# Performance work log

Measured on AMD Instinct MI355X. Metric: run time of the kernel, lower is better.

## Reference

```python
import jax, jax.numpy as jnp
import numpy as np

D_MODEL = 2048
N_HEADS = 16
D_HEAD = D_MODEL // N_HEADS
D_FF = 8192
EPS = 1e-6
ROPE_BASE = 10000.0


def rmsnorm(x, g):
    return x * jax.lax.rsqrt(jnp.mean(x * x, axis=-1, keepdims=True) + EPS) * g


def rotate_half(x):
    x1, x2 = jnp.split(x, 2, axis=-1)
    return jnp.concatenate((-x2, x1), axis=-1)


def rope_tables(T):
    inv_freq = 1.0 / (ROPE_BASE ** (jnp.arange(0, D_HEAD, 2, dtype=jnp.float32) / D_HEAD))
    freqs = jnp.arange(T, dtype=jnp.float32)[:, None] * inv_freq[None, :]  # [T, D_HEAD//2]
    emb = jnp.concatenate((freqs, freqs), axis=-1)  # [T, D_HEAD]
    return jnp.cos(emb), jnp.sin(emb)


def setup_inputs() -> dict:
    key = jax.random.key(0)
    ks = jax.random.split(key, 6)
    std = 0.02
    x = jax.random.normal(ks[0], (2, 2048, D_MODEL), dtype=jnp.float32)
    # weights stored (in, out) so forward is x @ W
    w_qkv = jax.random.normal(ks[1], (D_MODEL, 3 * D_MODEL), dtype=jnp.float32) * std
    w_out = jax.random.normal(ks[2], (D_MODEL, D_MODEL), dtype=jnp.float32) * std
    w_g = jax.random.normal(ks[3], (D_MODEL, D_FF), dtype=jnp.float32) * std
    w_u = jax.random.normal(ks[4], (D_MODEL, D_FF), dtype=jnp.float32) * std
    w_o = jax.random.normal(ks[5], (D_FF, D_MODEL), dtype=jnp.float32) * std
    g1 = jnp.ones((D_MODEL,), dtype=jnp.float32)
    g2 = jnp.ones((D_MODEL,), dtype=jnp.float32)
    return {"x": x, "w_qkv": w_qkv, "w_out": w_out, "g1": g1, "g2": g2,
            "w_g": w_g, "w_u": w_u, "w_o": w_o}


def reference(x, w_qkv, w_out, g1, g2, w_g, w_u, w_o):
    B, T, D = x.shape
    H, dh = N_HEADS, D_HEAD
    scale = dh ** -0.5

    h = rmsnorm(x, g1)
    qkv = h @ w_qkv  # [B, T, 3D]
    q, k, v = jnp.split(qkv, 3, axis=-1)
    # [B, H, T, dh]
    q = q.reshape(B, T, H, dh).transpose(0, 2, 1, 3)
    k = k.reshape(B, T, H, dh).transpose(0, 2, 1, 3)
    v = v.reshape(B, T, H, dh).transpose(0, 2, 1, 3)

    cos, sin = rope_tables(T)  # [T, dh] each
    cos = cos[None, None]
    sin = sin[None, None]
    q = q * cos + rotate_half(q) * sin
    k = k * cos + rotate_half(k) * sin

    scores = jnp.einsum('bhqd,bhkd->bhqk', q, k) * scale
    causal = jnp.arange(T)[None, :] <= jnp.arange(T)[:, None]  # [T, T]
    scores = jnp.where(causal[None, None], scores, -jnp.inf)
    attn = jax.nn.softmax(scores, axis=-1)
    ctx = jnp.einsum('bhqk,bhkd->bhqd', attn, v)  # [B, H, T, dh]
    ctx = ctx.transpose(0, 2, 1, 3).reshape(B, T, D)
    x = x + ctx @ w_out

    h = rmsnorm(x, g2)
    x = x + (jax.nn.silu(h @ w_g) * (h @ w_u)) @ w_o
    return x
```

## Files before the change

kernel.cpp:

```cpp
#include <hip/hip_runtime.h>

typedef __bf16 bf16x8 __attribute__((ext_vector_type(8)));
typedef float f32x4 __attribute__((ext_vector_type(4)));
typedef unsigned short u16x8 __attribute__((ext_vector_type(8)));

#define B_SZ 2
#define T_SEQ 2048
#define D_MODEL 2048
#define N_HEADS 16
#define D_HEAD 128
#define D_FF 8192
#define BT (B_SZ * T_SEQ)
#define NT (T_SEQ / 64)

__device__ __forceinline__ unsigned short f2bf(float f) {
  unsigned int u = __builtin_bit_cast(unsigned int, f);
  u += 0x7FFFu + ((u >> 16) & 1u);
  return (unsigned short)(u >> 16);
}
__device__ __forceinline__ float bf2f(unsigned short h) {
  unsigned int u = ((unsigned int)h) << 16;
  return __builtin_bit_cast(float, u);
}

__device__ __forceinline__ void load_lds16(const void* g, void* l) {
  __builtin_amdgcn_global_load_lds(
      (const __attribute__((address_space(1))) unsigned int*)g,
      (__attribute__((address_space(3))) unsigned int*)l, 16, 0, 0);
}

template <int N>
__device__ __forceinline__ void vm_gate() {
  if constexpr (N <= 0)
    asm volatile("s_waitcnt vmcnt(0)" ::: "memory");
  else if constexpr (N == 2)
    asm volatile("s_waitcnt vmcnt(2)" ::: "memory");
  else if constexpr (N == 3)
    asm volatile("s_waitcnt vmcnt(3)" ::: "memory");
  else if constexpr (N == 4)
    asm volatile("s_waitcnt vmcnt(4)" ::: "memory");
  else if constexpr (N == 6)
    asm volatile("s_waitcnt vmcnt(6)" ::: "memory");
  else
    asm volatile("s_waitcnt vmcnt(8)" ::: "memory");
}

__global__ __launch_bounds__(256) void transpose_cast_kernel(
    const float* __restrict__ in, unsigned short* __restrict__ out, int R, int C) {
  __shared__ float tile[32][33];
  const int tx = threadIdx.x, ty = threadIdx.y;
  const int c0 = blockIdx.x * 32, r0 = blockIdx.y * 32;
#pragma unroll
  for (int i = 0; i < 4; ++i)
    tile[ty + 8 * i][tx] = in[(long)(r0 + ty + 8 * i) * C + c0 + tx];
  __syncthreads();
#pragma unroll
  for (int i = 0; i < 4; ++i)
    out[(long)(c0 + ty + 8 * i) * R + r0 + tx] = f2bf(tile[tx][ty + 8 * i]);
}

__global__ __launch_bounds__(256) void rmsnorm_cast_kernel(
    const float* __restrict__ x, const float* __restrict__ gw,
    unsigned short* __restrict__ out) {
  const int row = blockIdx.x;
  const int tid = threadIdx.x;
  const float* xr = x + (long)row * D_MODEL;
  float4 a = *(const float4*)(xr + tid * 8);
  float4 b = *(const float4*)(xr + tid * 8 + 4);
  float ss = a.x * a.x + a.y * a.y + a.z * a.z + a.w * a.w +
             b.x * b.x + b.y * b.y + b.z * b.z + b.w * b.w;
#pragma unroll
  for (int d = 1; d < 64; d <<= 1) ss += __shfl_xor(ss, d);
  __shared__ float part[4];
  if ((tid & 63) == 0) part[tid >> 6] = ss;
  __syncthreads();
  ss = part[0] + part[1] + part[2] + part[3];
  const float rs = rsqrtf(ss * (1.0f / D_MODEL) + 1e-6f);
  float4 g0 = *(const float4*)(gw + tid * 8);
  float4 g1 = *(const float4*)(gw + tid * 8 + 4);
  ushort4 o0, o1;
  o0.x = f2bf(a.x * rs * g0.x); o0.y = f2bf(a.y * rs * g0.y);
  o0.z = f2bf(a.z * rs * g0.z); o0.w = f2bf(a.w * rs * g0.w);
  o1.x = f2bf(b.x * rs * g1.x); o1.y = f2bf(b.y * rs * g1.y);
  o1.z = f2bf(b.z * rs * g1.z); o1.w = f2bf(b.w * rs * g1.w);
  unsigned short* op = out + (long)row * D_MODEL + tid * 8;
  *(ushort4*)op = o0;
  *(ushort4*)(op + 4) = o1;
}

template <int EPI, int WM, int WN, int FM, int FN>
__global__ __launch_bounds__(WM * WN * 64, 2) void gemm_ks_kernel(
    const unsigned short* __restrict__ A, const unsigned short* __restrict__ Bt,
    void* __restrict__ Cout, const void* __restrict__ aux,
    int M, int N, int K, int lda, int ldb, int ldc, int cm, int cn) {
  constexpr int THREADS = WM * WN * 64;
  constexpr int BM = WM * FM * 16;
  constexpr int BN = WN * FN * 16;
  constexpr int ASLOT = BM * 32;
  constexpr int BSLOT = BN * 32;
  constexpr int RPR = THREADS / 4;
  constexpr int LPS = BM / RPR + BN / RPR;
  __shared__ unsigned short As[4 * ASLOT];
  __shared__ unsigned short Bs[4 * BSLOT];

  const int tid = threadIdx.x;
  const int lane = tid & 63, g = lane >> 4, c = lane & 15;
  const int w = tid >> 6, wr = w / WN, wc = w % WN;

  const int nbn = N / BN;
  const int bid = (int)blockIdx.x;
  const int xcd = bid & 7, idx = bid >> 3;
  const int chn = nbn / cn;
  const int crow = xcd / chn, ccol = xcd % chn;
  const int mr = idx / cn, nc2 = idx % cn;
  const int m0 = (crow * cm + mr) * BM;
  const int n0 = (ccol * cn + nc2) * BN;

  const int nks = K >> 5;
  const int srow = tid >> 2;
  const int kq8 = (tid & 3) * 8;
  const unsigned short* A_ = A + (long)m0 * lda;
  const unsigned short* B_ = Bt + (long)n0 * ldb;

  auto stage = [&](int s) {
    const int slot = s & 3;
    const long kofs = (long)s * 32 + kq8;
#pragma unroll
    for (int j = 0; j < BM / RPR; ++j)
      load_lds16(A_ + (long)(j * RPR + srow) * lda + kofs,
                 &As[slot * ASLOT + (j * THREADS + tid) * 8]);
#pragma unroll
    for (int j = 0; j < BN / RPR; ++j)
      load_lds16(B_ + (long)(j * RPR + srow) * ldb + kofs,
                 &Bs[slot * BSLOT + (j * THREADS + tid) * 8]);
  };

  f32x4 acc[FM][FN] = {};

  stage(0);
  if (nks > 1) stage(1);
  if (nks > 2) stage(2);
  vm_gate<2 * LPS>();
  __builtin_amdgcn_sched_barrier(0);
  __builtin_amdgcn_s_barrier();

  for (int s = 0; s < nks; ++s) {
    const int slot = s & 3;
    const unsigned short* Ap = &As[slot * ASLOT] + (wr * FM * 16 + c) * 32 + g * 8;
    const unsigned short* Bp = &Bs[slot * BSLOT] + (wc * FN * 16 + c) * 32 + g * 8;
    bf16x8 fa[FM], fb[FN];
#pragma unroll
    for (int fm = 0; fm < FM; ++fm) fa[fm] = *(const bf16x8*)(Ap + fm * 512);
#pragma unroll
    for (int fn = 0; fn < FN; ++fn) fb[fn] = *(const bf16x8*)(Bp + fn * 512);
    if (s + 3 < nks) stage(s + 3);
    __builtin_amdgcn_s_setprio(1);
#pragma unroll
    for (int fm = 0; fm < FM; ++fm)
#pragma unroll
      for (int fn = 0; fn < FN; ++fn)
        acc[fm][fn] = __builtin_amdgcn_mfma_f32_16x16x32_bf16(fa[fm], fb[fn], acc[fm][fn], 0, 0, 0);
    __builtin_amdgcn_s_setprio(0);
    if (s + 1 == nks) break;
    if (s <= nks - 4)
      vm_gate<2 * LPS>();
    else if (s == nks - 3)
      vm_gate<LPS>();
    else
      vm_gate<0>();
    __builtin_amdgcn_sched_barrier(0);
    __builtin_amdgcn_s_barrier();
  }

#pragma unroll
  for (int fm = 0; fm < FM; ++fm) {
#pragma unroll
    for (int r = 0; r < 4; ++r) {
      const int row = m0 + wr * FM * 16 + fm * 16 + 4 * g + r;
#pragma unroll
      for (int fn = 0; fn < FN; ++fn) {
        const int col = n0 + wc * FN * 16 + fn * 16 + c;
        const long idx2 = (long)row * ldc + col;
        float v = acc[fm][fn][r];
        if constexpr (EPI == 0) {
          ((unsigned short*)Cout)[idx2] = f2bf(v);
        } else if constexpr (EPI == 1) {
          ((float*)Cout)[idx2] = v + ((const float*)aux)[idx2];
        } else {
          const float u = bf2f(((const unsigned short*)aux)[idx2]);
          const float sg = v / (1.0f + __expf(-v));
          ((unsigned short*)Cout)[idx2] = f2bf(sg * u);
        }
      }
    }
  }
}

__global__ void rope_tables_kernel(float* __restrict__ cost, float* __restrict__ sint) {
  const int idx = blockIdx.x * 256 + threadIdx.x;
  const int t = idx >> 6, i = idx & 63;
  const float invf = powf(10000.0f, -(float)i * (1.0f / 64.0f));
  const float ang = (float)t * invf;
  cost[idx] = cosf(ang);
  sint[idx] = sinf(ang);
}

__global__ __launch_bounds__(256) void rope_apply_kernel(
    unsigned short* __restrict__ qkv, const float* __restrict__ cost,
    const float* __restrict__ sint) {
  const long idx = (long)blockIdx.x * 256 + threadIdx.x;
  const int i = idx & 63;
  const int h = (idx >> 6) & 15;
  const int qk = (idx >> 10) & 1;
  const int row = idx >> 11;
  const int t = row & (T_SEQ - 1);
  unsigned short* p = qkv + (long)row * (3 * D_MODEL) + qk * D_MODEL + h * D_HEAD + i;
  const float a = bf2f(p[0]);
  const float b = bf2f(p[64]);
  const float cv = cost[t * 64 + i];
  const float sv = sint[t * 64 + i];
  p[0] = f2bf(a * cv - b * sv);
  p[64] = f2bf(b * cv + a * sv);
}

__global__ __launch_bounds__(256) void vtrans_kernel(
    const unsigned short* __restrict__ qkv, unsigned short* __restrict__ vt) {
  __shared__ unsigned short tile[32][33];
  const int tx = threadIdx.x, ty = threadIdx.y;
  const int t0 = blockIdx.x * 32, d0 = blockIdx.y * 32;
  const int bh = blockIdx.z;
  const int b = bh >> 4, h = bh & 15;
#pragma unroll
  for (int i = 0; i < 4; ++i)
    tile[ty + 8 * i][tx] =
        qkv[(long)(b * T_SEQ + t0 + ty + 8 * i) * (3 * D_MODEL) + 2 * D_MODEL + h * D_HEAD + d0 + tx];
  __syncthreads();
#pragma unroll
  for (int i = 0; i < 4; ++i)
    vt[((long)bh * D_HEAD + d0 + ty + 8 * i) * T_SEQ + t0 + tx] = tile[tx][ty + 8 * i];
}

__global__ __launch_bounds__(256) void attn_kernel(
    const unsigned short* __restrict__ qkv, const unsigned short* __restrict__ vt,
    unsigned short* __restrict__ ctx) {
  __shared__ unsigned short Ks[2][64 * 128];
  __shared__ unsigned short Vs[2][128 * 64];
  const int h = blockIdx.y, b = blockIdx.z;
  const int tid = threadIdx.x;
  const int w = tid >> 6, lane = tid & 63, g = lane >> 4, c = lane & 15;
  const float scale = 0.08838834764831845f;
  const int srcA = (2 * (g & 1)) * 16 + c;
  const int srcB = srcA + 16;
  const bool hi = (g >> 1) != 0;
  const int bh = b * N_HEADS + h;

  const int ssk = (tid & 15) ^ ((tid >> 4) & 7);
  const int ssv = (tid & 7) ^ ((tid >> 3) & 7);
  const unsigned short* Kg = qkv + (long)b * T_SEQ * 3 * D_MODEL + D_MODEL + (long)h * D_HEAD;
  const unsigned short* Vg = vt + (long)bh * D_HEAD * T_SEQ;

  auto stage = [&](int kv0, int bufi) {
#pragma unroll
    for (int i = 0; i < 4; ++i) {
      const int rowk = i * 16 + (tid >> 4);
      load_lds16(Kg + (long)(kv0 + rowk) * (3 * D_MODEL) + ssk * 8,
                 &Ks[bufi][(i * 256 + tid) * 8]);
    }
#pragma unroll
    for (int i = 0; i < 4; ++i) {
      const int rowv = i * 32 + (tid >> 3);
      load_lds16(Vg + (long)rowv * T_SEQ + kv0 + ssv * 8,
                 &Vs[bufi][(i * 256 + tid) * 8]);
    }
  };

  const int cs7 = c & 7;

  for (int pass = 0; pass < 2; ++pass) {
    const int qt = pass ? (NT - 1 - blockIdx.x) : blockIdx.x;
    const int q = qt * 64 + w * 16 + c;

    bf16x8 fq[4];
    const long rowQ = (long)(b * T_SEQ + q) * (3 * D_MODEL) + h * D_HEAD;
#pragma unroll
    for (int ks = 0; ks < 4; ++ks)
      fq[ks] = *(const bf16x8*)(qkv + rowQ + ks * 32 + g * 8);

    f32x4 o[8] = {};
    float mrun = -INFINITY, ell = 0.0f;

    stage(0, 0);
    asm volatile("s_waitcnt vmcnt(0)" ::: "memory");
    __syncthreads();
    int buf = 0;

    for (int kt = 0; kt <= qt; ++kt) {
      const int kv0 = kt * 64;
      if (kt < qt) stage(kv0 + 64, buf ^ 1);

      f32x4 s[4] = {};
#pragma unroll
      for (int fm = 0; fm < 4; ++fm) {
        const unsigned short* kr = &Ks[buf][(fm * 16 + c) * 128];
#pragma unroll
        for (int ks = 0; ks < 4; ++ks) {
          bf16x8 ak = *(const bf16x8*)(kr + ((ks * 4 + g) ^ cs7) * 8);
          s[fm] = __builtin_amdgcn_mfma_f32_16x16x32_bf16(ak, fq[ks], s[fm], 0, 0, 0);
        }
      }
      float pmax = -INFINITY;
      const bool diag = (kt == qt);
#pragma unroll
      for (int fm = 0; fm < 4; ++fm)
#pragma unroll
        for (int r = 0; r < 4; ++r) {
          float sv = s[fm][r] * scale;
          if (diag) {
            const int kp = kv0 + fm * 16 + 4 * g + r;
            if (kp > q) sv = -INFINITY;
          }
          s[fm][r] = sv;
          pmax = fmaxf(pmax, sv);
        }
      pmax = fmaxf(pmax, __shfl_xor(pmax, 16));
      pmax = fmaxf(pmax, __shfl_xor(pmax, 32));
      const float mnew = fmaxf(mrun, pmax);
      const float resc = __expf(mrun - mnew);
      mrun = mnew;
      float rowsum = 0.0f;
#pragma unroll
      for (int fm = 0; fm < 4; ++fm)
#pragma unroll
        for (int r = 0; r < 4; ++r) {
          const float p = __expf(s[fm][r] - mnew);
          s[fm][r] = p;
          rowsum += p;
        }
      rowsum += __shfl_xor(rowsum, 16);
      rowsum += __shfl_xor(rowsum, 32);
      ell = ell * resc + rowsum;
#pragma unroll
      for (int fm = 0; fm < 8; ++fm) o[fm] *= resc;

      bf16x8 pb[2];
#pragma unroll
      for (int k2 = 0; k2 < 2; ++k2) {
        float va[4], vb[4];
#pragma unroll
        for (int r = 0; r < 4; ++r) {
          const float t0 = __shfl(s[k2 * 2][r], srcA);
          const float t1 = __shfl(s[k2 * 2 + 1][r], srcA);
          va[r] = hi ? t1 : t0;
          const float u0 = __shfl(s[k2 * 2][r], srcB);
          const float u1 = __shfl(s[k2 * 2 + 1][r], srcB);
          vb[r] = hi ? u1 : u0;
        }
        bf16x8 pv;
        pv[0] = (__bf16)va[0]; pv[1] = (__bf16)va[1];
        pv[2] = (__bf16)va[2]; pv[3] = (__bf16)va[3];
        pv[4] = (__bf16)vb[0]; pv[5] = (__bf16)vb[1];
        pv[6] = (__bf16)vb[2]; pv[7] = (__bf16)vb[3];
        pb[k2] = pv;
      }
#pragma unroll
      for (int fm = 0; fm < 8; ++fm) {
        const unsigned short* vr = &Vs[buf][(fm * 16 + c) * 64];
#pragma unroll
        for (int k2 = 0; k2 < 2; ++k2) {
          bf16x8 av = *(const bf16x8*)(vr + ((k2 * 4 + g) ^ cs7) * 8);
          o[fm] = __builtin_amdgcn_mfma_f32_16x16x32_bf16(av, pb[k2], o[fm], 0, 0, 0);
        }
      }
      asm volatile("s_waitcnt vmcnt(0)" ::: "memory");
      __syncthreads();
      buf ^= 1;
    }

    const float inv = 1.0f / ell;
    unsigned short* outp = ctx + (long)(b * T_SEQ + q) * D_MODEL + h * D_HEAD;
#pragma unroll
    for (int fm = 0; fm < 8; ++fm) {
      ushort4 pk;
      pk.x = f2bf(o[fm][0] * inv);
      pk.y = f2bf(o[fm][1] * inv);
      pk.z = f2bf(o[fm][2] * inv);
      pk.w = f2bf(o[fm][3] * inv);
      *(ushort4*)(outp + fm * 16 + 4 * g) = pk;
    }
  }
}

extern "C" void kernel_launch(void* const* d_in, const int* in_sizes, int n_in,
                              void* d_out, int out_size, void* d_ws, size_t ws_size,
                              hipStream_t stream) {
  const float* x = (const float*)d_in[0];
  const float* w_qkv = (const float*)d_in[1];
  const float* w_out = (const float*)d_in[2];
  const float* g1 = (const float*)d_in[3];
  const float* g2 = (const float*)d_in[4];
  const float* w_g = (const float*)d_in[5];
  const float* w_u = (const float*)d_in[6];
  const float* w_o = (const float*)d_in[7];
  float* out = (float*)d_out;

  char* ws = (char*)d_ws;
  size_t off = 0;
  auto take = [&](size_t bytes) {
    char* p = ws + off;
    off += (bytes + 255) & ~(size_t)255;
    return p;
  };

  char* Wreg = take((size_t)3 * D_FF * D_MODEL * 2);
  unsigned short* wTqkv = (unsigned short*)Wreg;
  unsigned short* wTout = (unsigned short*)(Wreg + (size_t)3 * D_MODEL * D_MODEL * 2);
  unsigned short* wTg = (unsigned short*)Wreg;
  unsigned short* wTu = (unsigned short*)(Wreg + (size_t)D_FF * D_MODEL * 2);
  unsigned short* wTo = (unsigned short*)(Wreg + (size_t)2 * D_FF * D_MODEL * 2);

  const size_t qkv_b = (size_t)BT * 3 * D_MODEL * 2;
  const size_t vt_b = (size_t)B_SZ * N_HEADS * D_HEAD * T_SEQ * 2;
  const size_t ctx_b = (size_t)BT * D_MODEL * 2;
  char* AR = take(qkv_b + vt_b + ctx_b);
  unsigned short* qkvb = (unsigned short*)AR;
  unsigned short* vtb = (unsigned short*)(AR + qkv_b);
  unsigned short* ctxb = (unsigned short*)(AR + qkv_b + vt_b);
  unsigned short* gbuf = (unsigned short*)AR;
  unsigned short* ubuf = (unsigned short*)(AR + (size_t)BT * (D_FF / 2) * 2);

  float* x1 = (float*)take((size_t)BT * D_MODEL * 4);
  unsigned short* hb = (unsigned short*)take((size_t)BT * D_MODEL * 2);
  float* cost = (float*)take((size_t)T_SEQ * 64 * 4);
  float* sint = (float*)take((size_t)T_SEQ * 64 * 4);

  const dim3 tb(32, 8);

  transpose_cast_kernel<<<dim3(3 * D_MODEL / 32, D_MODEL / 32), tb, 0, stream>>>(w_qkv, wTqkv, D_MODEL, 3 * D_MODEL);
  transpose_cast_kernel<<<dim3(D_MODEL / 32, D_MODEL / 32), tb, 0, stream>>>(w_out, wTout, D_MODEL, D_MODEL);
  rope_tables_kernel<<<T_SEQ * 64 / 256, 256, 0, stream>>>(cost, sint);

  rmsnorm_cast_kernel<<<BT, 256, 0, stream>>>(x, g1, hb);
  gemm_ks_kernel<0, 2, 4, 8, 4><<<384, 512, 0, stream>>>(
      hb, wTqkv, qkvb, nullptr, BT, 3 * D_MODEL, D_MODEL, D_MODEL, D_MODEL, 3 * D_MODEL, 8, 6);
  rope_apply_kernel<<<(BT * N_HEADS * 64 * 2) / 256, 256, 0, stream>>>(qkvb, cost, sint);
  vtrans_kernel<<<dim3(T_SEQ / 32, D_HEAD / 32, B_SZ * N_HEADS), tb, 0, stream>>>(qkvb, vtb);
  attn_kernel<<<dim3(NT / 2, N_HEADS, B_SZ), 256, 0, stream>>>(qkvb, vtb, ctxb);
  gemm_ks_kernel<1, 4, 2, 4, 4><<<256, 512, 0, stream>>>(
      ctxb, wTout, x1, x, BT, D_MODEL, D_MODEL, D_MODEL, D_MODEL, D_MODEL, 8, 4);

  transpose_cast_kernel<<<dim3(D_FF / 32, D_MODEL / 32), tb, 0, stream>>>(w_g, wTg, D_MODEL, D_FF);
  transpose_cast_kernel<<<dim3(D_FF / 32, D_MODEL / 32), tb, 0, stream>>>(w_u, wTu, D_MODEL, D_FF);
  transpose_cast_kernel<<<dim3(D_MODEL / 32, D_FF / 32), tb, 0, stream>>>(w_o, wTo, D_FF, D_MODEL);
  rmsnorm_cast_kernel<<<BT, 256, 0, stream>>>(x1, g2, hb);

  const int NH = D_FF / 2;
  for (int half = 0; half < 2; ++half) {
    const unsigned short* wTu_h = wTu + (size_t)half * NH * D_MODEL;
    const unsigned short* wTg_h = wTg + (size_t)half * NH * D_MODEL;
    const unsigned short* wTo_h = wTo + (size_t)half * NH;
    gemm_ks_kernel<0, 2, 4, 8, 4><<<256, 512, 0, stream>>>(
        hb, wTu_h, ubuf, nullptr, BT, NH, D_MODEL, D_MODEL, D_MODEL, NH, 4, 8);
    gemm_ks_kernel<2, 2, 4, 8, 4><<<256, 512, 0, stream>>>(
        hb, wTg_h, gbuf, ubuf, BT, NH, D_MODEL, D_MODEL, D_MODEL, NH, 4, 8);
    gemm_ks_kernel<1, 4, 2, 4, 4><<<256, 512, 0, stream>>>(
        gbuf, wTo_h, out, (half == 0) ? x1 : out, BT, D_MODEL, NH, NH, D_FF, D_MODEL, 8, 4);
  }
}
```

Before: 803.6 us.

## Merge two down-projection GEMMs into one dual-A K=8192 pass; add MFMA setprio in attention

```diff
diff --git a/kernel.cpp b/kernel.cpp
--- a/kernel.cpp
+++ b/kernel.cpp
@@ -88,10 +88,11 @@
   *(ushort4*)(op + 4) = o1;
 }
 
-template <int EPI, int WM, int WN, int FM, int FN>
+template <int EPI, int WM, int WN, int FM, int FN, bool DUALA = false>
 __global__ __launch_bounds__(WM * WN * 64, 2) void gemm_ks_kernel(
     const unsigned short* __restrict__ A, const unsigned short* __restrict__ Bt,
     void* __restrict__ Cout, const void* __restrict__ aux,
+    const unsigned short* __restrict__ A2,
     int M, int N, int K, int lda, int ldb, int ldc, int cm, int cn) {
   constexpr int THREADS = WM * WN * 64;
   constexpr int BM = WM * FM * 16;
@@ -120,18 +121,31 @@
   const int srow = tid >> 2;
   const int kq8 = (tid & 3) * 8;
   const unsigned short* A_ = A + (long)m0 * lda;
+  const unsigned short* A2_ = DUALA ? (A2 + (long)m0 * lda) : nullptr;
   const unsigned short* B_ = Bt + (long)n0 * ldb;
 
   auto stage = [&](int s) {
     const int slot = s & 3;
-    const long kofs = (long)s * 32 + kq8;
+    const long k32 = (long)s * 32;
+    const unsigned short* Ab;
+    long akofs;
+    if constexpr (DUALA) {
+      const int khalf = K >> 1;
+      const bool lo = k32 < khalf;
+      Ab = lo ? A_ : A2_;
+      akofs = (lo ? k32 : k32 - khalf) + kq8;
+    } else {
+      Ab = A_;
+      akofs = k32 + kq8;
+    }
+    const long bkofs = k32 + kq8;
 #pragma unroll
     for (int j = 0; j < BM / RPR; ++j)
-      load_lds16(A_ + (long)(j * RPR + srow) * lda + kofs,
+      load_lds16(Ab + (long)(j * RPR + srow) * lda + akofs,
                  &As[slot * ASLOT + (j * THREADS + tid) * 8]);
 #pragma unroll
     for (int j = 0; j < BN / RPR; ++j)
-      load_lds16(B_ + (long)(j * RPR + srow) * ldb + kofs,
+      load_lds16(B_ + (long)(j * RPR + srow) * ldb + bkofs,
                  &Bs[slot * BSLOT + (j * THREADS + tid) * 8]);
   };
 
@@ -299,6 +313,7 @@
       if (kt < qt) stage(kv0 + 64, buf ^ 1);
 
       f32x4 s[4] = {};
+      __builtin_amdgcn_s_setprio(1);
 #pragma unroll
       for (int fm = 0; fm < 4; ++fm) {
         const unsigned short* kr = &Ks[buf][(fm * 16 + c) * 128];
@@ -308,6 +323,7 @@
           s[fm] = __builtin_amdgcn_mfma_f32_16x16x32_bf16(ak, fq[ks], s[fm], 0, 0, 0);
         }
       }
+      __builtin_amdgcn_s_setprio(0);
       float pmax = -INFINITY;
       const bool diag = (kt == qt);
 #pragma unroll
@@ -362,6 +378,7 @@
         pv[6] = (__bf16)vb[2]; pv[7] = (__bf16)vb[3];
         pb[k2] = pv;
       }
+      __builtin_amdgcn_s_setprio(1);
 #pragma unroll
       for (int fm = 0; fm < 8; ++fm) {
         const unsigned short* vr = &Vs[buf][(fm * 16 + c) * 64];
@@ -371,6 +388,7 @@
           o[fm] = __builtin_amdgcn_mfma_f32_16x16x32_bf16(av, pb[k2], o[fm], 0, 0, 0);
         }
       }
+      __builtin_amdgcn_s_setprio(0);
       asm volatile("s_waitcnt vmcnt(0)" ::: "memory");
       __syncthreads();
       buf ^= 1;
@@ -425,8 +443,8 @@
   unsigned short* qkvb = (unsigned short*)AR;
   unsigned short* vtb = (unsigned short*)(AR + qkv_b);
   unsigned short* ctxb = (unsigned short*)(AR + qkv_b + vt_b);
-  unsigned short* gbuf = (unsigned short*)AR;
-  unsigned short* ubuf = (unsigned short*)(AR + (size_t)BT * (D_FF / 2) * 2);
+  unsigned short* gbuf0 = (unsigned short*)AR;
+  unsigned short* gbuf1 = (unsigned short*)(AR + (size_t)BT * (D_FF / 2) * 2);
 
   float* x1 = (float*)take((size_t)BT * D_MODEL * 4);
   unsigned short* hb = (unsigned short*)take((size_t)BT * D_MODEL * 2);
@@ -441,12 +459,12 @@
 
   rmsnorm_cast_kernel<<<BT, 256, 0, stream>>>(x, g1, hb);
   gemm_ks_kernel<0, 2, 4, 8, 4><<<384, 512, 0, stream>>>(
-      hb, wTqkv, qkvb, nullptr, BT, 3 * D_MODEL, D_MODEL, D_MODEL, D_MODEL, 3 * D_MODEL, 8, 6);
+      hb, wTqkv, qkvb, nullptr, nullptr, BT, 3 * D_MODEL, D_MODEL, D_MODEL, D_MODEL, 3 * D_MODEL, 8, 6);
   rope_apply_kernel<<<(BT * N_HEADS * 64 * 2) / 256, 256, 0, stream>>>(qkvb, cost, sint);
   vtrans_kernel<<<dim3(T_SEQ / 32, D_HEAD / 32, B_SZ * N_HEADS), tb, 0, stream>>>(qkvb, vtb);
   attn_kernel<<<dim3(NT / 2, N_HEADS, B_SZ), 256, 0, stream>>>(qkvb, vtb, ctxb);
   gemm_ks_kernel<1, 4, 2, 4, 4><<<256, 512, 0, stream>>>(
-      ctxb, wTout, x1, x, BT, D_MODEL, D_MODEL, D_MODEL, D_MODEL, D_MODEL, 8, 4);
+      ctxb, wTout, x1, x, nullptr, BT, D_MODEL, D_MODEL, D_MODEL, D_MODEL, D_MODEL, 8, 4);
 
   transpose_cast_kernel<<<dim3(D_FF / 32, D_MODEL / 32), tb, 0, stream>>>(w_g, wTg, D_MODEL, D_FF);
   transpose_cast_kernel<<<dim3(D_FF / 32, D_MODEL / 32), tb, 0, stream>>>(w_u, wTu, D_MODEL, D_FF);
@@ -457,12 +475,12 @@
   for (int half = 0; half < 2; ++half) {
     const unsigned short* wTu_h = wTu + (size_t)half * NH * D_MODEL;
     const unsigned short* wTg_h = wTg + (size_t)half * NH * D_MODEL;
-    const unsigned short* wTo_h = wTo + (size_t)half * NH;
+    unsigned short* gb = half ? gbuf1 : gbuf0;
     gemm_ks_kernel<0, 2, 4, 8, 4><<<256, 512, 0, stream>>>(
-        hb, wTu_h, ubuf, nullptr, BT, NH, D_MODEL, D_MODEL, D_MODEL, NH, 4, 8);
+        hb, wTu_h, gb, nullptr, nullptr, BT, NH, D_MODEL, D_MODEL, D_MODEL, NH, 4, 8);
     gemm_ks_kernel<2, 2, 4, 8, 4><<<256, 512, 0, stream>>>(
-        hb, wTg_h, gbuf, ubuf, BT, NH, D_MODEL, D_MODEL, D_MODEL, NH, 4, 8);
-    gemm_ks_kernel<1, 4, 2, 4, 4><<<256, 512, 0, stream>>>(
-        gbuf, wTo_h, out, (half == 0) ? x1 : out, BT, D_MODEL, NH, NH, D_FF, D_MODEL, 8, 4);
+        hb, wTg_h, gb, gb, nullptr, BT, NH, D_MODEL, D_MODEL, D_MODEL, NH, 4, 8);
   }
-}
+  gemm_ks_kernel<1, 4, 2, 4, 4, true><<<256, 512, 0, stream>>>(
+      gbuf0, wTo, out, x1, gbuf1, BT, D_MODEL, D_FF, NH, D_FF, D_MODEL, 8, 4);
+}
```

Measured after the change: 793.5 us. About the same (-1.3%).
